# Optimization experiments

Measured on AMD Instinct MI355X. Metric: run time of the kernel, lower is better.

## Reference

```python
import jax, jax.numpy as jnp
import numpy as np

N, E = 50000, 800000
IN = OUT = 128
T, R, H = 4, 6, 8
DK = OUT // H


def setup_inputs() -> dict:
    key = jax.random.key(0)
    ks = iter(jax.random.split(key, 24))
    nk = lambda: next(ks)
    return {
        "node_inp": jax.random.normal(nk(), (N, IN), jnp.float32),
        "node_type": jax.random.randint(nk(), (N,), 0, T),
        "edge_index": jax.random.randint(nk(), (2, E), 0, N),
        "edge_type": jax.random.randint(nk(), (E,), 0, R),
        "edge_sign": jax.random.randint(nk(), (E,), -2, 2),
        "edge_distance": jax.random.uniform(nk(), (E,), jnp.float32, 0.0, 2e5),
        "Wq": jax.random.normal(nk(), (T, IN, OUT), jnp.float32) / np.float32(np.sqrt(IN)),
        "bq": jnp.zeros((T, OUT), jnp.float32),
        "Wk": jax.random.normal(nk(), (T, IN, OUT), jnp.float32) / np.float32(np.sqrt(IN)),
        "bk": jnp.zeros((T, OUT), jnp.float32),
        "Wv": jax.random.normal(nk(), (T, IN, OUT), jnp.float32) / np.float32(np.sqrt(IN)),
        "bv": jnp.zeros((T, OUT), jnp.float32),
        "rel_q": jax.random.normal(nk(), (R, H, DK), jnp.float32) * 0.2,
        "rel_k": jax.random.normal(nk(), (R, H, DK), jnp.float32) * 0.2,
        "rel_v": jax.random.normal(nk(), (R, H, DK), jnp.float32) * 0.2,
        "sign_k_neutral": jnp.ones((H, DK), jnp.float32),
        "sign_v_neutral": jnp.ones((H, DK), jnp.float32),
        "rel_bias": jnp.zeros((R, H), jnp.float32),
        "dist_alpha": jnp.asarray(0.5, jnp.float32),
        "dist_tau": jnp.asarray(100000.0, jnp.float32),
        "skip": jnp.ones((T,), jnp.float32),
        "ln_gamma": jnp.ones((T, OUT), jnp.float32),
        "ln_beta": jnp.zeros((T, OUT), jnp.float32),
    }


def reference(node_inp, node_type, edge_index, edge_type, edge_sign, edge_distance,
              Wq, bq, Wk, bk, Wv, bv, rel_q, rel_k, rel_v,
              sign_k_neutral, sign_v_neutral, rel_bias, dist_alpha, dist_tau,
              skip, ln_gamma, ln_beta):
    n = node_inp.shape[0]
    src, dst = edge_index[0], edge_index[1]

    # edge_sign normalization: anything < -1 or == 0 -> -2 (neutral), else clamp to {-1, 1}
    es = jnp.where((edge_sign < -1) | (edge_sign == 0), -2, jnp.clip(edge_sign, -1, 1))
    sign_idx = jnp.where(es == -1, 0, jnp.where(es == 1, 1, 2))  # [E]

    # per-type Q/K/V projections, then select by node_type
    idx = jnp.arange(n)
    Q = (jnp.einsum('ni,tio->tno', node_inp, Wq) + bq[:, None, :])[node_type, idx]
    K = (jnp.einsum('ni,tio->tno', node_inp, Wk) + bk[:, None, :])[node_type, idx]
    V = (jnp.einsum('ni,tio->tno', node_inp, Wv) + bv[:, None, :])[node_type, idx]
    Q = Q.reshape(n, H, DK); K = K.reshape(n, H, DK); V = V.reshape(n, H, DK)

    sign_k_all = jnp.concatenate([-jnp.ones((1, H, DK), Q.dtype), jnp.ones((1, H, DK), Q.dtype), sign_k_neutral[None]], 0)
    sign_v_all = jnp.concatenate([-jnp.ones((1, H, DK), Q.dtype), jnp.ones((1, H, DK), Q.dtype), sign_v_neutral[None]], 0)

    q_eff = Q[dst] * rel_q[edge_type]                        # [E,H,DK]
    k_eff = K[src] * rel_k[edge_type] * sign_k_all[sign_idx]  # [E,H,DK]
    v_eff = V[src] * rel_v[edge_type] * sign_v_all[sign_idx]  # [E,H,DK]

    scores = (q_eff * k_eff).sum(-1) / np.float32(np.sqrt(DK))  # [E,H]
    scores = scores + rel_bias[edge_type]
    phi = dist_alpha * jnp.exp(-edge_distance / (dist_tau + 1e-9))
    scores = scores + phi[:, None]

    # destination-grouped softmax over edges
    m = jax.ops.segment_max(scores, dst, num_segments=n)      # [N,H]
    ex = jnp.exp(scores - m[dst])
    Z = jax.ops.segment_sum(ex, dst, num_segments=n)          # [N,H]
    attn = ex / (Z[dst] + 1e-9)                               # [E,H]

    msg = (v_eff * attn[..., None]).reshape(-1, OUT)          # [E,OUT]
    out = jax.ops.segment_sum(msg, dst, num_segments=n)       # [N,OUT]

    alpha = jax.nn.sigmoid(skip)[node_type][:, None]          # [N,1]
    mix = alpha * out + (1.0 - alpha) * node_inp
    mu = mix.mean(-1, keepdims=True)
    var = ((mix - mu) ** 2).mean(-1, keepdims=True)
    normed = (mix - mu) / jnp.sqrt(var + 1e-5)
    return normed * ln_gamma[node_type] + ln_beta[node_type]
```

## Files before the change

### kernel.cpp

```cpp
#include <hip/hip_runtime.h>

#define N_NODES 50000
#define N_EDGES 800000
#define DIM 128
#define NT 4
#define NR 6
#define NH 8
#define NBLK_SCAN ((N_NODES + 255) / 256)
#define NTILE_ROW 3129
#define NPAD_MAX (NTILE_ROW * 16)

#define XCVT_N (N_NODES * DIM / 4)
#define WT_N   (NT * 3 * DIM * DIM)
#define WCB_N  (24 * 32)
#define PREP_TOTAL (XCVT_N + WT_N + WCB_N)
#define PREP_BLOCKS ((PREP_TOTAL + 255) / 256)
#define HIST_BLOCKS (N_EDGES / 256)
#define MID_PREP_BASE NBLK_SCAN
#define MID_HIST_BASE (NBLK_SCAN + PREP_BLOCKS)
#define MID_BLOCKS (MID_HIST_BASE + HIST_BLOCKS)

typedef __attribute__((ext_vector_type(8))) short bf16x8;
typedef __attribute__((ext_vector_type(4))) float f32x4;

__device__ __forceinline__ unsigned short f2bf(float f) {
    unsigned int u = __float_as_uint(f);
    return (unsigned short)((u + 0x7fffu + ((u >> 16) & 1u)) >> 16);
}
__device__ __forceinline__ float blo(unsigned int u) { return __uint_as_float(u << 16); }
__device__ __forceinline__ float bhi(unsigned int u) { return __uint_as_float(u & 0xffff0000u); }

__device__ __forceinline__ int sign_index(int s) {
    if (s < -1 || s == 0) return 2;
    return (s == -1) ? 0 : 1;
}

__global__ __launch_bounds__(256) void k_typehist(const int* __restrict__ ntype,
                                                  int* __restrict__ bhist,
                                                  int* __restrict__ cnt,
                                                  int* __restrict__ opad) {
    __shared__ int h[NT];
    if (threadIdx.x < NT) h[threadIdx.x] = 0;
    __syncthreads();
    int n = blockIdx.x * 256 + threadIdx.x;
    if (n < N_NODES) { atomicAdd(&h[ntype[n]], 1); cnt[n] = 0; }
    if (n < NPAD_MAX) opad[n] = -1;
    __syncthreads();
    if (threadIdx.x < NT) bhist[blockIdx.x * NT + threadIdx.x] = h[threadIdx.x];
}

__global__ __launch_bounds__(1024) void k_typescan(const int* __restrict__ bhist,
                                                   int* __restrict__ bbase,
                                                   int* __restrict__ pb_g) {
    __shared__ int s[1024];
    __shared__ int pb[NT + 1];
    int tid = threadIdx.x;
    int t = tid / NBLK_SCAN;
    int b = tid - t * NBLK_SCAN;
    int v = (tid < NT * NBLK_SCAN) ? bhist[b * NT + t] : 0;
    s[tid] = v;
    __syncthreads();
    for (int d = 1; d < 1024; d <<= 1) {
        int add = (tid >= d) ? s[tid - d] : 0;
        __syncthreads();
        s[tid] += add;
        __syncthreads();
    }
    if (tid == 0) {
        int acc = 0;
        for (int tt = 0; tt < NT; ++tt) {
            pb[tt] = acc;
            int tot = s[(tt + 1) * NBLK_SCAN - 1] - (tt ? s[tt * NBLK_SCAN - 1] : 0);
            acc += ((tot + 15) >> 4) << 4;
        }
        pb[NT] = acc;
    }
    __syncthreads();
    if (tid < NT * NBLK_SCAN) {
        int excl = s[tid] - v;
        int base_t = t ? s[t * NBLK_SCAN - 1] : 0;
        bbase[b * NT + t] = pb[t] + (excl - base_t);
    }
    if (tid <= NT) pb_g[tid] = pb[tid];
}

__global__ __launch_bounds__(256) void k_mid(
    const int* __restrict__ ntype, const int* __restrict__ bbase, int* __restrict__ order_pad,
    const float* __restrict__ x,
    const float* __restrict__ Wq, const float* __restrict__ Wk, const float* __restrict__ Wv,
    const float* __restrict__ rel_q, const float* __restrict__ rel_k,
    const float* __restrict__ rel_v,
    const float* __restrict__ skn, const float* __restrict__ svn,
    unsigned short* __restrict__ xb, unsigned short* __restrict__ Wt,
    uint4* __restrict__ wcb,
    const int* __restrict__ ei, int* __restrict__ cnt, int* __restrict__ posw)
{
    int blk = blockIdx.x;
    if (blk < NBLK_SCAN) {
        __shared__ int cur[NT];
        if (threadIdx.x < NT) cur[threadIdx.x] = bbase[blk * NT + threadIdx.x];
        __syncthreads();
        int n = blk * 256 + threadIdx.x;
        if (n < N_NODES) {
            int t = ntype[n];
            int pos = atomicAdd(&cur[t], 1);
            order_pad[pos] = n;
        }
        return;
    }
    if (blk < MID_HIST_BASE) {
        int i = (blk - MID_PREP_BASE) * 256 + threadIdx.x;
        if (i < XCVT_N) {
            float4 v = ((const float4*)x)[i];
            ushort4 o;
            o.x = f2bf(v.x); o.y = f2bf(v.y); o.z = f2bf(v.z); o.w = f2bf(v.w);
            ((ushort4*)xb)[i] = o;
        } else if (i < XCVT_N + WT_N) {
            int j = i - XCVT_N;
            int in = j & 127;
            int b2 = j >> 7;
            int out = b2 & 127;
            int ts = b2 >> 7;
            int sel = ts % 3, t = ts / 3;
            const float* W = sel == 0 ? Wq : (sel == 1 ? Wk : Wv);
            Wt[j] = f2bf(W[((size_t)t * DIM + in) * DIM + out]);
        } else if (i < PREP_TOTAL) {
            int j = i - XCVT_N - WT_N;
            int p = j & 31;
            int cmb = j >> 5;
            int et = cmb & 7, sidx = cmb >> 3;
            if (et < NR) {
                int h = p >> 2;
                float wk[4], wv[4];
                #pragma unroll
                for (int q = 0; q < 4; ++q) {
                    int o = 4 * p + q;
                    int rb = (et * NH + h) * 16 + (o & 15);
                    float sgk = sidx == 0 ? -1.f : (sidx == 1 ? 1.f : skn[o]);
                    float sgv = sidx == 0 ? -1.f : (sidx == 1 ? 1.f : svn[o]);
                    wk[q] = rel_q[rb] * rel_k[rb] * sgk * 0.25f;
                    wv[q] = rel_v[rb] * sgv;
                }
                uint4 u;
                u.x = (unsigned)f2bf(wk[0]) | ((unsigned)f2bf(wk[1]) << 16);
                u.y = (unsigned)f2bf(wv[0]) | ((unsigned)f2bf(wv[1]) << 16);
                u.z = (unsigned)f2bf(wk[2]) | ((unsigned)f2bf(wk[3]) << 16);
                u.w = (unsigned)f2bf(wv[2]) | ((unsigned)f2bf(wv[3]) << 16);
                wcb[cmb * 32 + p] = u;
            }
        }
        return;
    }
    int e = (blk - MID_HIST_BASE) * 256 + threadIdx.x;
    if (e < N_EDGES) posw[e] = atomicAdd(&cnt[ei[N_EDGES + e]], 1);
}

__global__ __launch_bounds__(256) void k_projm(
    const unsigned short* __restrict__ xb, const unsigned short* __restrict__ Wt,
    const int* __restrict__ order_pad, const int* __restrict__ pb_g,
    const float* __restrict__ bq, const float* __restrict__ bk, const float* __restrict__ bv,
    float* __restrict__ Qf, unsigned short* __restrict__ KVu,
    const int* __restrict__ cnt, int* __restrict__ offs, int* __restrict__ bsum)
{
    int b = blockIdx.x;
    if (b >= NTILE_ROW) {
        int sb = b - NTILE_ROW;
        __shared__ int s[256];
        int i = sb * 256 + threadIdx.x;
        int v = (i < N_NODES) ? cnt[i] : 0;
        s[threadIdx.x] = v;
        __syncthreads();
        for (int d = 1; d < 256; d <<= 1) {
            int add = (threadIdx.x >= d) ? s[threadIdx.x - d] : 0;
            __syncthreads();
            s[threadIdx.x] += add;
            __syncthreads();
        }
        if (i < N_NODES) offs[i] = s[threadIdx.x] - v;
        if (threadIdx.x == 255) bsum[sb] = s[255];
        return;
    }
    int row0 = b * 16;
    if (row0 >= pb_g[NT]) return;
    int t = (row0 >= pb_g[3]) ? 3 : (row0 >= pb_g[2]) ? 2 : (row0 >= pb_g[1]) ? 1 : 0;
    int wave = threadIdx.x >> 6, lane = threadIdx.x & 63;
    int arow = row0 + (lane & 15);
    int nidA = order_pad[arow];
    const unsigned short* xrow = xb + (size_t)(nidA < 0 ? 0 : nidA) * DIM;
    int ko = (lane >> 4) * 8;
    bf16x8 afrag[4];
    #pragma unroll
    for (int kt = 0; kt < 4; ++kt) afrag[kt] = *(const bf16x8*)(xrow + kt * 32 + ko);

    #pragma unroll
    for (int g = 0; g < 6; ++g) {
        int ocol = g * 64 + wave * 16 + (lane & 15);
        int sel = ocol >> 7, wcol = ocol & 127;
        const unsigned short* wrow = Wt + ((size_t)(t * 3 + sel) * DIM + wcol) * DIM;
        f32x4 acc = {0.f, 0.f, 0.f, 0.f};
        #pragma unroll
        for (int kt = 0; kt < 4; ++kt) {
            bf16x8 bfr = *(const bf16x8*)(wrow + kt * 32 + ko);
            acc = __builtin_amdgcn_mfma_f32_16x16x32_bf16(afrag[kt], bfr, acc, 0, 0, 0);
        }
        const float* bias_p = sel == 0 ? bq : (sel == 1 ? bk : bv);
        float bias = bias_p[t * DIM + wcol];
        #pragma unroll
        for (int r = 0; r < 4; ++r) {
            int drow = row0 + (lane >> 4) * 4 + r;
            int nid = order_pad[drow];
            if (nid < 0) continue;
            float v = acc[r] + bias;
            if (sel == 0) Qf[(size_t)nid * DIM + wcol] = v;
            else KVu[(size_t)nid * 256 + (wcol >> 1) * 4 + (wcol & 1) + (sel == 2 ? 2 : 0)] = f2bf(v);
        }
    }
}

__global__ __launch_bounds__(256) void k_scan2(const int* __restrict__ bsum,
                                               int* __restrict__ bofs, int* __restrict__ offs) {
    __shared__ int s[256];
    int t = threadIdx.x;
    int v = (t < NBLK_SCAN) ? bsum[t] : 0;
    s[t] = v;
    __syncthreads();
    for (int d = 1; d < 256; d <<= 1) {
        int add = (t >= d) ? s[t - d] : 0;
        __syncthreads();
        s[t] += add;
        __syncthreads();
    }
    if (t < NBLK_SCAN) {
        int b = s[t] - v;
        bofs[t] = b;
        if (t == NBLK_SCAN - 1) offs[N_NODES] = N_EDGES - b;
    }
}

__global__ void k_emit(const int* __restrict__ ei, const int* __restrict__ etype,
                       const int* __restrict__ esign, const float* __restrict__ edist,
                       const float* __restrict__ dalpha, const float* __restrict__ dtau,
                       const int* __restrict__ offs, const int* __restrict__ bofs,
                       const int* __restrict__ posw, int2* __restrict__ edata) {
    int e = blockIdx.x * blockDim.x + threadIdx.x;
    if (e >= N_EDGES) return;
    int dst = ei[N_EDGES + e];
    int pos = offs[dst] + bofs[dst >> 8] + posw[e];
    int cmb = sign_index(esign[e]) * 8 + etype[e];
    float phi = dalpha[0] * __expf(-edist[e] / (dtau[0] + 1e-9f));
    edata[pos] = make_int2(ei[e] | (cmb << 16), __float_as_int(phi));
}

__global__ __launch_bounds__(256) void k_attn(
    const float4* __restrict__ Qf4, const uint4* __restrict__ KV,
    const uint4* __restrict__ WCB,
    const float* __restrict__ x, const int* __restrict__ ntype,
    const int* __restrict__ offs, const int* __restrict__ bofs,
    const int2* __restrict__ edata,
    const float* __restrict__ rbias, const float* __restrict__ skip,
    const float* __restrict__ gmm, const float* __restrict__ bta,
    float* __restrict__ out)
{
    __shared__ float rb_s[NR * NH];
    if (threadIdx.x < NR * NH) rb_s[threadIdx.x] = rbias[threadIdx.x];
    __syncthreads();
    const int wave = threadIdx.x >> 6, lane = threadIdx.x & 63;
    const int n = blockIdx.x * 4 + wave;
    const int p = lane & 31;
    const int hi = lane >> 5;
    const int h = p >> 2;
    const int beg = offs[n] + bofs[n >> 8];
    const int end = offs[n + 1] + bofs[(n + 1) >> 8];

    const float4 q4 = Qf4[(size_t)n * 32 + p];

    float Z = 0.f, a0 = 0.f, a1 = 0.f, a2 = 0.f, a3 = 0.f;

    auto process = [&](int2 r) {
        int src = r.x & 0xffff;
        unsigned cmb = ((unsigned)r.x) >> 16;
        uint4 kv = KV[(size_t)src * 32 + p];
        uint4 w = WCB[cmb * 32 + p];
        float pp = (q4.x * blo(w.x)) * blo(kv.x);
        pp = fmaf(q4.y * bhi(w.x), bhi(kv.x), pp);
        pp = fmaf(q4.z * blo(w.z), blo(kv.z), pp);
        pp = fmaf(q4.w * bhi(w.z), bhi(kv.z), pp);
        pp += __shfl_xor(pp, 1, 4);
        pp += __shfl_xor(pp, 2, 4);
        float ex = __expf(pp + rb_s[(cmb & 7) * NH + h] + __int_as_float(r.y));
        Z += ex;
        a0 = fmaf(blo(kv.y) * blo(w.y), ex, a0);
        a1 = fmaf(bhi(kv.y) * bhi(w.y), ex, a1);
        a2 = fmaf(blo(kv.w) * blo(w.w), ex, a2);
        a3 = fmaf(bhi(kv.w) * bhi(w.w), ex, a3);
    };

    int rem = end - beg;
    int j = beg;
    if (rem >= 4) {
        int2 r0 = edata[j + hi];
        int2 r1 = edata[j + 2 + hi];
        while (true) {
            int2 c0 = r0, c1 = r1;
            j += 4; rem -= 4;
            if (rem >= 4) { r0 = edata[j + hi]; r1 = edata[j + 2 + hi]; }
            process(c0);
            process(c1);
            if (rem < 4) break;
        }
    }
    while (rem >= 2) {
        int2 c = edata[j + hi];
        process(c);
        j += 2; rem -= 2;
    }
    if (rem) {
        int2 r = edata[j];
        int src = r.x & 0xffff;
        unsigned cmb = ((unsigned)r.x) >> 16;
        uint4 kv = KV[(size_t)src * 32 + p];
        uint4 w = WCB[cmb * 32 + p];
        float pp = (q4.x * blo(w.x)) * blo(kv.x);
        pp = fmaf(q4.y * bhi(w.x), bhi(kv.x), pp);
        pp = fmaf(q4.z * blo(w.z), blo(kv.z), pp);
        pp = fmaf(q4.w * bhi(w.z), bhi(kv.z), pp);
        pp += __shfl_xor(pp, 1, 4);
        pp += __shfl_xor(pp, 2, 4);
        float ex = __expf(pp + rb_s[(cmb & 7) * NH + h] + __int_as_float(r.y));
        ex = hi ? 0.f : ex;
        Z += ex;
        a0 = fmaf(blo(kv.y) * blo(w.y), ex, a0);
        a1 = fmaf(bhi(kv.y) * bhi(w.y), ex, a1);
        a2 = fmaf(blo(kv.w) * blo(w.w), ex, a2);
        a3 = fmaf(bhi(kv.w) * bhi(w.w), ex, a3);
    }

    Z  += __shfl_xor(Z, 32, 64);
    a0 += __shfl_xor(a0, 32, 64);
    a1 += __shfl_xor(a1, 32, 64);
    a2 += __shfl_xor(a2, 32, 64);
    a3 += __shfl_xor(a3, 32, 64);

    float rz = 1.f / (Z + 1e-9f);
    int t = ntype[n];
    float alpha = 1.f / (1.f + __expf(-skip[t]));
    float4 x4 = ((const float4*)x)[(size_t)n * 32 + p];
    float m0 = fmaf(alpha, a0 * rz - x4.x, x4.x);
    float m1 = fmaf(alpha, a1 * rz - x4.y, x4.y);
    float m2 = fmaf(alpha, a2 * rz - x4.z, x4.z);
    float m3 = fmaf(alpha, a3 * rz - x4.w, x4.w);

    float s = (m0 + m1) + (m2 + m3);
    float s2 = fmaf(m0, m0, m1 * m1) + fmaf(m2, m2, m3 * m3);
    #pragma unroll
    for (int d = 32; d >= 1; d >>= 1) {
        s += __shfl_xor(s, d, 64);
        s2 += __shfl_xor(s2, d, 64);
    }
    float mu = s * (1.f / (2 * DIM));
    float var = s2 * (1.f / (2 * DIM)) - mu * mu;
    float rstd = rsqrtf(var + 1e-5f);
    if (hi == 0) {
        float4 g4 = ((const float4*)gmm)[t * 32 + p];
        float4 b4 = ((const float4*)bta)[t * 32 + p];
        float4 o4;
        o4.x = (m0 - mu) * rstd * g4.x + b4.x;
        o4.y = (m1 - mu) * rstd * g4.y + b4.y;
        o4.z = (m2 - mu) * rstd * g4.z + b4.z;
        o4.w = (m3 - mu) * rstd * g4.w + b4.w;
        ((float4*)out)[(size_t)n * 32 + p] = o4;
    }
}

extern "C" void kernel_launch(void* const* d_in, const int* in_sizes, int n_in,
                              void* d_out, int out_size, void* d_ws, size_t ws_size,
                              hipStream_t stream) {
    const float* x      = (const float*)d_in[0];
    const int*   ntype  = (const int*)d_in[1];
    const int*   ei     = (const int*)d_in[2];
    const int*   etype  = (const int*)d_in[3];
    const int*   esign  = (const int*)d_in[4];
    const float* edist  = (const float*)d_in[5];
    const float* Wq     = (const float*)d_in[6];
    const float* bq     = (const float*)d_in[7];
    const float* Wk     = (const float*)d_in[8];
    const float* bk     = (const float*)d_in[9];
    const float* Wv     = (const float*)d_in[10];
    const float* bv     = (const float*)d_in[11];
    const float* rel_q  = (const float*)d_in[12];
    const float* rel_k  = (const float*)d_in[13];
    const float* rel_v  = (const float*)d_in[14];
    const float* skn    = (const float*)d_in[15];
    const float* svn    = (const float*)d_in[16];
    const float* rbias  = (const float*)d_in[17];
    const float* dalpha = (const float*)d_in[18];
    const float* dtau   = (const float*)d_in[19];
    const float* skip   = (const float*)d_in[20];
    const float* gmm    = (const float*)d_in[21];
    const float* bta    = (const float*)d_in[22];
    float* out = (float*)d_out;

    char* ws = (char*)d_ws;
    float*          Qf     = (float*)         (ws + 0);
    unsigned short* KVu    = (unsigned short*)(ws + 25600000);
    unsigned short* xb     = (unsigned short*)(ws + 51200000);
    unsigned short* Wt     = (unsigned short*)(ws + 64000000);
    uint4*          wcb    = (uint4*)         (ws + 64500000);
    int*            cnt    = (int*)           (ws + 64600000);
    int*            offs   = (int*)           (ws + 64900000);
    int*            bsum   = (int*)           (ws + 65200000);
    int*            bofs   = (int*)           (ws + 65210000);
    int*            posw   = (int*)           (ws + 65300000);
    int2*           edata  = (int2*)          (ws + 68600000);
    int*            opad   = (int*)           (ws + 75000000);
    int*            bhist  = (int*)           (ws + 75300000);
    int*            bbase  = (int*)           (ws + 75310000);
    int*            pb     = (int*)           (ws + 75320000);

    k_typehist <<<NBLK_SCAN, 256, 0, stream>>>(ntype, bhist, cnt, opad);
    k_typescan <<<1, 1024, 0, stream>>>(bhist, bbase, pb);
    k_mid <<<MID_BLOCKS, 256, 0, stream>>>(ntype, bbase, opad,
                                           x, Wq, Wk, Wv, rel_q, rel_k, rel_v, skn, svn,
                                           xb, Wt, wcb,
                                           ei, cnt, posw);
    k_projm <<<NTILE_ROW + NBLK_SCAN, 256, 0, stream>>>(xb, Wt, opad, pb, bq, bk, bv,
                                                        Qf, KVu, cnt, offs, bsum);
    k_scan2 <<<1, 256, 0, stream>>>(bsum, bofs, offs);
    k_emit <<<HIST_BLOCKS, 256, 0, stream>>>(ei, etype, esign, edist, dalpha, dtau,
                                             offs, bofs, posw, edata);
    k_attn <<<N_NODES / 4, 256, 0, stream>>>((const float4*)Qf, (const uint4*)KVu,
                                             (const uint4*)wcb, x, ntype, offs, bofs,
                                             edata, rbias, skip, gmm, bta, out);
}
```

Baseline: 182.8 us.

## Prefetch gathered KV rows in attention loop, split relation weights to fp32, restructure projection GEMM

The attention kernel now issues the gathered KV and relation-weight loads for the next pair of edges before processing the current pair, so memory latency overlaps with compute. The combined relation/sign weight table is split into separate fp32 K and V tables, which removes bf16 unpacking but doubles that table's footprint and load count. The projection GEMM is reorganized so each block owns one output-column group and loops over a chunk of 8 row tiles. Weight fragments are reused across tiles and reloaded only when the node type changes, while x rows are now re-read for each of the 6 column groups.

```diff
diff --git a/kernel.cpp b/kernel.cpp
--- a/kernel.cpp
+++ b/kernel.cpp
@@ -9,6 +9,9 @@
 #define NBLK_SCAN ((N_NODES + 255) / 256)
 #define NTILE_ROW 3129
 #define NPAD_MAX (NTILE_ROW * 16)
+#define CHUNK 8
+#define NCHUNK ((NTILE_ROW + CHUNK - 1) / CHUNK)
+#define GEMM_BLOCKS (NCHUNK * 6)
 
 #define XCVT_N (N_NODES * DIM / 4)
 #define WT_N   (NT * 3 * DIM * DIM)
@@ -92,7 +95,7 @@
     const float* __restrict__ rel_v,
     const float* __restrict__ skn, const float* __restrict__ svn,
     unsigned short* __restrict__ xb, unsigned short* __restrict__ Wt,
-    uint4* __restrict__ wcb,
+    float4* __restrict__ wcbK, float4* __restrict__ wcbV,
     const int* __restrict__ ei, int* __restrict__ cnt, int* __restrict__ posw)
 {
     int blk = blockIdx.x;
@@ -141,12 +144,8 @@
                     wk[q] = rel_q[rb] * rel_k[rb] * sgk * 0.25f;
                     wv[q] = rel_v[rb] * sgv;
                 }
-                uint4 u;
-                u.x = (unsigned)f2bf(wk[0]) | ((unsigned)f2bf(wk[1]) << 16);
-                u.y = (unsigned)f2bf(wv[0]) | ((unsigned)f2bf(wv[1]) << 16);
-                u.z = (unsigned)f2bf(wk[2]) | ((unsigned)f2bf(wk[3]) << 16);
-                u.w = (unsigned)f2bf(wv[2]) | ((unsigned)f2bf(wv[3]) << 16);
-                wcb[cmb * 32 + p] = u;
+                wcbK[cmb * 32 + p] = make_float4(wk[0], wk[1], wk[2], wk[3]);
+                wcbV[cmb * 32 + p] = make_float4(wv[0], wv[1], wv[2], wv[3]);
             }
         }
         return;
@@ -163,8 +162,8 @@
     const int* __restrict__ cnt, int* __restrict__ offs, int* __restrict__ bsum)
 {
     int b = blockIdx.x;
-    if (b >= NTILE_ROW) {
-        int sb = b - NTILE_ROW;
+    if (b >= GEMM_BLOCKS) {
+        int sb = b - GEMM_BLOCKS;
         __shared__ int s[256];
         int i = sb * 256 + threadIdx.x;
         int v = (i < N_NODES) ? cnt[i] : 0;
@@ -180,31 +179,38 @@
         if (threadIdx.x == 255) bsum[sb] = s[255];
         return;
     }
-    int row0 = b * 16;
-    if (row0 >= pb_g[NT]) return;
-    int t = (row0 >= pb_g[3]) ? 3 : (row0 >= pb_g[2]) ? 2 : (row0 >= pb_g[1]) ? 1 : 0;
+    int chunk = b / 6, g = b % 6;
     int wave = threadIdx.x >> 6, lane = threadIdx.x & 63;
-    int arow = row0 + (lane & 15);
-    int nidA = order_pad[arow];
-    const unsigned short* xrow = xb + (size_t)(nidA < 0 ? 0 : nidA) * DIM;
+    int ocol = g * 64 + wave * 16 + (lane & 15);
+    int sel = ocol >> 7, wcol = ocol & 127;
     int ko = (lane >> 4) * 8;
-    bf16x8 afrag[4];
-    #pragma unroll
-    for (int kt = 0; kt < 4; ++kt) afrag[kt] = *(const bf16x8*)(xrow + kt * 32 + ko);
-
-    #pragma unroll
-    for (int g = 0; g < 6; ++g) {
-        int ocol = g * 64 + wave * 16 + (lane & 15);
-        int sel = ocol >> 7, wcol = ocol & 127;
-        const unsigned short* wrow = Wt + ((size_t)(t * 3 + sel) * DIM + wcol) * DIM;
+    const float* bias_p = sel == 0 ? bq : (sel == 1 ? bk : bv);
+    int cur_t = -1;
+    bf16x8 bfr[4];
+    float bias = 0.f;
+    int tile0 = chunk * CHUNK;
+    int tmax = pb_g[NT];
+    #pragma unroll 1
+    for (int tt = 0; tt < CHUNK; ++tt) {
+        int row0 = (tile0 + tt) * 16;
+        if (row0 >= tmax) break;
+        int t = (row0 >= pb_g[3]) ? 3 : (row0 >= pb_g[2]) ? 2 : (row0 >= pb_g[1]) ? 1 : 0;
+        if (t != cur_t) {
+            cur_t = t;
+            const unsigned short* wrow = Wt + ((size_t)(t * 3 + sel) * DIM + wcol) * DIM;
+            #pragma unroll
+            for (int kt = 0; kt < 4; ++kt) bfr[kt] = *(const bf16x8*)(wrow + kt * 32 + ko);
+            bias = bias_p[t * DIM + wcol];
+        }
+        int arow = row0 + (lane & 15);
+        int nidA = order_pad[arow];
+        const unsigned short* xrow = xb + (size_t)(nidA < 0 ? 0 : nidA) * DIM;
         f32x4 acc = {0.f, 0.f, 0.f, 0.f};
         #pragma unroll
         for (int kt = 0; kt < 4; ++kt) {
-            bf16x8 bfr = *(const bf16x8*)(wrow + kt * 32 + ko);
-            acc = __builtin_amdgcn_mfma_f32_16x16x32_bf16(afrag[kt], bfr, acc, 0, 0, 0);
-        }
-        const float* bias_p = sel == 0 ? bq : (sel == 1 ? bk : bv);
-        float bias = bias_p[t * DIM + wcol];
+            bf16x8 a = *(const bf16x8*)(xrow + kt * 32 + ko);
+            acc = __builtin_amdgcn_mfma_f32_16x16x32_bf16(a, bfr[kt], acc, 0, 0, 0);
+        }
         #pragma unroll
         for (int r = 0; r < 4; ++r) {
             int drow = row0 + (lane >> 4) * 4 + r;
@@ -253,7 +259,7 @@
 
 __global__ __launch_bounds__(256) void k_attn(
     const float4* __restrict__ Qf4, const uint4* __restrict__ KV,
-    const uint4* __restrict__ WCB,
+    const float4* __restrict__ WK, const float4* __restrict__ WV,
     const float* __restrict__ x, const int* __restrict__ ntype,
     const int* __restrict__ offs, const int* __restrict__ bofs,
     const int2* __restrict__ edata,
@@ -276,63 +282,77 @@
 
     float Z = 0.f, a0 = 0.f, a1 = 0.f, a2 = 0.f, a3 = 0.f;
 
-    auto process = [&](int2 r) {
-        int src = r.x & 0xffff;
-        unsigned cmb = ((unsigned)r.x) >> 16;
-        uint4 kv = KV[(size_t)src * 32 + p];
-        uint4 w = WCB[cmb * 32 + p];
-        float pp = (q4.x * blo(w.x)) * blo(kv.x);
-        pp = fmaf(q4.y * bhi(w.x), bhi(kv.x), pp);
-        pp = fmaf(q4.z * blo(w.z), blo(kv.z), pp);
-        pp = fmaf(q4.w * bhi(w.z), bhi(kv.z), pp);
+    auto PROC = [&](int2 r, uint4 kv, float4 wk, float4 wv) {
+        float pp = (q4.x * wk.x) * blo(kv.x);
+        pp = fmaf(q4.y * wk.y, bhi(kv.x), pp);
+        pp = fmaf(q4.z * wk.z, blo(kv.z), pp);
+        pp = fmaf(q4.w * wk.w, bhi(kv.z), pp);
         pp += __shfl_xor(pp, 1, 4);
         pp += __shfl_xor(pp, 2, 4);
+        unsigned cmb = ((unsigned)r.x) >> 16;
         float ex = __expf(pp + rb_s[(cmb & 7) * NH + h] + __int_as_float(r.y));
         Z += ex;
-        a0 = fmaf(blo(kv.y) * blo(w.y), ex, a0);
-        a1 = fmaf(bhi(kv.y) * bhi(w.y), ex, a1);
-        a2 = fmaf(blo(kv.w) * blo(w.w), ex, a2);
-        a3 = fmaf(bhi(kv.w) * bhi(w.w), ex, a3);
+        a0 = fmaf(blo(kv.y) * wv.x, ex, a0);
+        a1 = fmaf(bhi(kv.y) * wv.y, ex, a1);
+        a2 = fmaf(blo(kv.w) * wv.z, ex, a2);
+        a3 = fmaf(bhi(kv.w) * wv.w, ex, a3);
     };
 
     int rem = end - beg;
     int j = beg;
     if (rem >= 4) {
-        int2 r0 = edata[j + hi];
-        int2 r1 = edata[j + 2 + hi];
-        while (true) {
-            int2 c0 = r0, c1 = r1;
+        int2 r0 = edata[j + hi], r1 = edata[j + 2 + hi];
+        uint4  kv0 = KV[(size_t)(r0.x & 0xffff) * 32 + p];
+        float4 wk0 = WK[(((unsigned)r0.x) >> 16) * 32 + p];
+        float4 wv0 = WV[(((unsigned)r0.x) >> 16) * 32 + p];
+        uint4  kv1 = KV[(size_t)(r1.x & 0xffff) * 32 + p];
+        float4 wk1 = WK[(((unsigned)r1.x) >> 16) * 32 + p];
+        float4 wv1 = WV[(((unsigned)r1.x) >> 16) * 32 + p];
+        while (rem >= 8) {
+            int2 n0 = edata[j + 4 + hi], n1 = edata[j + 6 + hi];
+            uint4  nkv0 = KV[(size_t)(n0.x & 0xffff) * 32 + p];
+            float4 nwk0 = WK[(((unsigned)n0.x) >> 16) * 32 + p];
+            float4 nwv0 = WV[(((unsigned)n0.x) >> 16) * 32 + p];
+            uint4  nkv1 = KV[(size_t)(n1.x & 0xffff) * 32 + p];
+            float4 nwk1 = WK[(((unsigned)n1.x) >> 16) * 32 + p];
+            float4 nwv1 = WV[(((unsigned)n1.x) >> 16) * 32 + p];
+            PROC(r0, kv0, wk0, wv0);
+            PROC(r1, kv1, wk1, wv1);
+            r0 = n0; kv0 = nkv0; wk0 = nwk0; wv0 = nwv0;
+            r1 = n1; kv1 = nkv1; wk1 = nwk1; wv1 = nwv1;
             j += 4; rem -= 4;
-            if (rem >= 4) { r0 = edata[j + hi]; r1 = edata[j + 2 + hi]; }
-            process(c0);
-            process(c1);
-            if (rem < 4) break;
-        }
+        }
+        PROC(r0, kv0, wk0, wv0);
+        PROC(r1, kv1, wk1, wv1);
+        j += 4; rem -= 4;
     }
     while (rem >= 2) {
-        int2 c = edata[j + hi];
-        process(c);
+        int2 r = edata[j + hi];
+        uint4  kv = KV[(size_t)(r.x & 0xffff) * 32 + p];
+        float4 wk = WK[(((unsigned)r.x) >> 16) * 32 + p];
+        float4 wv = WV[(((unsigned)r.x) >> 16) * 32 + p];
+        PROC(r, kv, wk, wv);
         j += 2; rem -= 2;
     }
     if (rem) {
         int2 r = edata[j];
-        int src = r.x & 0xffff;
-        unsigned cmb = ((unsigned)r.x) >> 16;
-        uint4 kv = KV[(size_t)src * 32 + p];
-        uint4 w = WCB[cmb * 32 + p];
-        float pp = (q4.x * blo(w.x)) * blo(kv.x);
-        pp = fmaf(q4.y * bhi(w.x), bhi(kv.x), pp);
-        pp = fmaf(q4.z * blo(w.z), blo(kv.z), pp);
-        pp = fmaf(q4.w * bhi(w.z), bhi(kv.z), pp);
+        uint4  kv = KV[(size_t)(r.x & 0xffff) * 32 + p];
+        float4 wk = WK[(((unsigned)r.x) >> 16) * 32 + p];
+        float4 wv = WV[(((unsigned)r.x) >> 16) * 32 + p];
+        float pp = (q4.x * wk.x) * blo(kv.x);
+        pp = fmaf(q4.y * wk.y, bhi(kv.x), pp);
+        pp = fmaf(q4.z * wk.z, blo(kv.z), pp);
+        pp = fmaf(q4.w * wk.w, bhi(kv.z), pp);
         pp += __shfl_xor(pp, 1, 4);
         pp += __shfl_xor(pp, 2, 4);
+        unsigned cmb = ((unsigned)r.x) >> 16;
         float ex = __expf(pp + rb_s[(cmb & 7) * NH + h] + __int_as_float(r.y));
         ex = hi ? 0.f : ex;
         Z += ex;
-        a0 = fmaf(blo(kv.y) * blo(w.y), ex, a0);
-        a1 = fmaf(bhi(kv.y) * bhi(w.y), ex, a1);
-        a2 = fmaf(blo(kv.w) * blo(w.w), ex, a2);
-        a3 = fmaf(bhi(kv.w) * bhi(w.w), ex, a3);
+        a0 = fmaf(blo(kv.y) * wv.x, ex, a0);
+        a1 = fmaf(bhi(kv.y) * wv.y, ex, a1);
+        a2 = fmaf(blo(kv.w) * wv.z, ex, a2);
+        a3 = fmaf(bhi(kv.w) * wv.w, ex, a3);
     }
 
     Z  += __shfl_xor(Z, 32, 64);
@@ -405,7 +425,8 @@
     unsigned short* KVu    = (unsigned short*)(ws + 25600000);
     unsigned short* xb     = (unsigned short*)(ws + 51200000);
     unsigned short* Wt     = (unsigned short*)(ws + 64000000);
-    uint4*          wcb    = (uint4*)         (ws + 64500000);
+    float4*         wcbK   = (float4*)        (ws + 64500000);
+    float4*         wcbV   = (float4*)        (ws + 64520000);
     int*            cnt    = (int*)           (ws + 64600000);
     int*            offs   = (int*)           (ws + 64900000);
     int*            bsum   = (int*)           (ws + 65200000);
@@ -421,14 +442,15 @@
     k_typescan <<<1, 1024, 0, stream>>>(bhist, bbase, pb);
     k_mid <<<MID_BLOCKS, 256, 0, stream>>>(ntype, bbase, opad,
                                            x, Wq, Wk, Wv, rel_q, rel_k, rel_v, skn, svn,
-                                           xb, Wt, wcb,
+                                           xb, Wt, wcbK, wcbV,
                                            ei, cnt, posw);
-    k_projm <<<NTILE_ROW + NBLK_SCAN, 256, 0, stream>>>(xb, Wt, opad, pb, bq, bk, bv,
-                                                        Qf, KVu, cnt, offs, bsum);
+    k_projm <<<GEMM_BLOCKS + NBLK_SCAN, 256, 0, stream>>>(xb, Wt, opad, pb, bq, bk, bv,
+                                                          Qf, KVu, cnt, offs, bsum);
     k_scan2 <<<1, 256, 0, stream>>>(bsum, bofs, offs);
     k_emit <<<HIST_BLOCKS, 256, 0, stream>>>(ei, etype, esign, edist, dalpha, dtau,
                                              offs, bofs, posw, edata);
     k_attn <<<N_NODES / 4, 256, 0, stream>>>((const float4*)Qf, (const uint4*)KVu,
-                                             (const uint4*)wcb, x, ntype, offs, bofs,
+                                             (const float4*)wcbK, (const float4*)wcbV,
+                                             x, ntype, offs, bofs,
                                              edata, rbias, skip, gmm, bta, out);
 }
```

After: 199.2 us. 1.09x slower.

## Regroup preprocessing stages into fewer fused launches to cut kernel launch count

Applied to the files above, without the earlier changes.

Restructures the preprocessing pipeline so independent stages share launches: the type histogram joins the conversion/edge-count kernel, the type scan and per-node offset scan share one kernel, the type scatter and block-sum scan share another, and the edge emit runs alongside the projection GEMM. The node-count scan switches to 1024-thread blocks so the second-level scan covers fewer blocks, and the count buffer is cleared with a memset. This is meant to remove launch gaps and tiny serial kernels, at the cost of more heterogeneous blocks within each launch.

```diff
diff --git a/kernel.cpp b/kernel.cpp
--- a/kernel.cpp
+++ b/kernel.cpp
@@ -7,6 +7,7 @@
 #define NR 6
 #define NH 8
 #define NBLK_SCAN ((N_NODES + 255) / 256)
+#define NBLK2 ((N_NODES + 1023) / 1024)
 #define NTILE_ROW 3129
 #define NPAD_MAX (NTILE_ROW * 16)
 
@@ -16,9 +17,9 @@
 #define PREP_TOTAL (XCVT_N + WT_N + WCB_N)
 #define PREP_BLOCKS ((PREP_TOTAL + 255) / 256)
 #define HIST_BLOCKS (N_EDGES / 256)
-#define MID_PREP_BASE NBLK_SCAN
-#define MID_HIST_BASE (NBLK_SCAN + PREP_BLOCKS)
-#define MID_BLOCKS (MID_HIST_BASE + HIST_BLOCKS)
+#define A_PREP_BASE NBLK_SCAN
+#define A_HIST_BASE (NBLK_SCAN + PREP_BLOCKS)
+#define A_BLOCKS (A_HIST_BASE + HIST_BLOCKS)
 
 typedef __attribute__((ext_vector_type(8))) short bf16x8;
 typedef __attribute__((ext_vector_type(4))) float f32x4;
@@ -35,57 +36,8 @@
     return (s == -1) ? 0 : 1;
 }
 
-__global__ __launch_bounds__(256) void k_typehist(const int* __restrict__ ntype,
-                                                  int* __restrict__ bhist,
-                                                  int* __restrict__ cnt,
-                                                  int* __restrict__ opad) {
-    __shared__ int h[NT];
-    if (threadIdx.x < NT) h[threadIdx.x] = 0;
-    __syncthreads();
-    int n = blockIdx.x * 256 + threadIdx.x;
-    if (n < N_NODES) { atomicAdd(&h[ntype[n]], 1); cnt[n] = 0; }
-    if (n < NPAD_MAX) opad[n] = -1;
-    __syncthreads();
-    if (threadIdx.x < NT) bhist[blockIdx.x * NT + threadIdx.x] = h[threadIdx.x];
-}
-
-__global__ __launch_bounds__(1024) void k_typescan(const int* __restrict__ bhist,
-                                                   int* __restrict__ bbase,
-                                                   int* __restrict__ pb_g) {
-    __shared__ int s[1024];
-    __shared__ int pb[NT + 1];
-    int tid = threadIdx.x;
-    int t = tid / NBLK_SCAN;
-    int b = tid - t * NBLK_SCAN;
-    int v = (tid < NT * NBLK_SCAN) ? bhist[b * NT + t] : 0;
-    s[tid] = v;
-    __syncthreads();
-    for (int d = 1; d < 1024; d <<= 1) {
-        int add = (tid >= d) ? s[tid - d] : 0;
-        __syncthreads();
-        s[tid] += add;
-        __syncthreads();
-    }
-    if (tid == 0) {
-        int acc = 0;
-        for (int tt = 0; tt < NT; ++tt) {
-            pb[tt] = acc;
-            int tot = s[(tt + 1) * NBLK_SCAN - 1] - (tt ? s[tt * NBLK_SCAN - 1] : 0);
-            acc += ((tot + 15) >> 4) << 4;
-        }
-        pb[NT] = acc;
-    }
-    __syncthreads();
-    if (tid < NT * NBLK_SCAN) {
-        int excl = s[tid] - v;
-        int base_t = t ? s[t * NBLK_SCAN - 1] : 0;
-        bbase[b * NT + t] = pb[t] + (excl - base_t);
-    }
-    if (tid <= NT) pb_g[tid] = pb[tid];
-}
-
-__global__ __launch_bounds__(256) void k_mid(
-    const int* __restrict__ ntype, const int* __restrict__ bbase, int* __restrict__ order_pad,
+__global__ __launch_bounds__(256) void k_A(
+    const int* __restrict__ ntype, int* __restrict__ bhist, int* __restrict__ opad,
     const float* __restrict__ x,
     const float* __restrict__ Wq, const float* __restrict__ Wk, const float* __restrict__ Wv,
     const float* __restrict__ rel_q, const float* __restrict__ rel_k,
@@ -97,19 +49,18 @@
 {
     int blk = blockIdx.x;
     if (blk < NBLK_SCAN) {
-        __shared__ int cur[NT];
-        if (threadIdx.x < NT) cur[threadIdx.x] = bbase[blk * NT + threadIdx.x];
+        __shared__ int h[NT];
+        if (threadIdx.x < NT) h[threadIdx.x] = 0;
         __syncthreads();
         int n = blk * 256 + threadIdx.x;
-        if (n < N_NODES) {
-            int t = ntype[n];
-            int pos = atomicAdd(&cur[t], 1);
-            order_pad[pos] = n;
-        }
+        if (n < N_NODES) atomicAdd(&h[ntype[n]], 1);
+        if (n < NPAD_MAX) opad[n] = -1;
+        __syncthreads();
+        if (threadIdx.x < NT) bhist[blk * NT + threadIdx.x] = h[threadIdx.x];
         return;
     }
-    if (blk < MID_HIST_BASE) {
-        int i = (blk - MID_PREP_BASE) * 256 + threadIdx.x;
+    if (blk < A_HIST_BASE) {
+        int i = (blk - A_PREP_BASE) * 256 + threadIdx.x;
         if (i < XCVT_N) {
             float4 v = ((const float4*)x)[i];
             ushort4 o;
@@ -130,12 +81,12 @@
             int cmb = j >> 5;
             int et = cmb & 7, sidx = cmb >> 3;
             if (et < NR) {
-                int h = p >> 2;
+                int h2 = p >> 2;
                 float wk[4], wv[4];
                 #pragma unroll
                 for (int q = 0; q < 4; ++q) {
                     int o = 4 * p + q;
-                    int rb = (et * NH + h) * 16 + (o & 15);
+                    int rb = (et * NH + h2) * 16 + (o & 15);
                     float sgk = sidx == 0 ? -1.f : (sidx == 1 ? 1.f : skn[o]);
                     float sgv = sidx == 0 ? -1.f : (sidx == 1 ? 1.f : svn[o]);
                     wk[q] = rel_q[rb] * rel_k[rb] * sgk * 0.25f;
@@ -151,33 +102,118 @@
         }
         return;
     }
-    int e = (blk - MID_HIST_BASE) * 256 + threadIdx.x;
+    int e = (blk - A_HIST_BASE) * 256 + threadIdx.x;
     if (e < N_EDGES) posw[e] = atomicAdd(&cnt[ei[N_EDGES + e]], 1);
 }
 
-__global__ __launch_bounds__(256) void k_projm(
+__global__ __launch_bounds__(1024) void k_B(
+    const int* __restrict__ bhist, int* __restrict__ bbase, int* __restrict__ pb_g,
+    const int* __restrict__ cnt, int* __restrict__ offs, int* __restrict__ bsum)
+{
+    int tid = threadIdx.x;
+    if (blockIdx.x == 0) {
+        __shared__ int s[1024];
+        __shared__ int pb[NT + 1];
+        int t = tid / NBLK_SCAN;
+        int b = tid - t * NBLK_SCAN;
+        int v = (tid < NT * NBLK_SCAN) ? bhist[b * NT + t] : 0;
+        s[tid] = v;
+        __syncthreads();
+        for (int d = 1; d < 1024; d <<= 1) {
+            int add = (tid >= d) ? s[tid - d] : 0;
+            __syncthreads();
+            s[tid] += add;
+            __syncthreads();
+        }
+        if (tid == 0) {
+            int acc = 0;
+            for (int tt = 0; tt < NT; ++tt) {
+                pb[tt] = acc;
+                int tot = s[(tt + 1) * NBLK_SCAN - 1] - (tt ? s[tt * NBLK_SCAN - 1] : 0);
+                acc += ((tot + 15) >> 4) << 4;
+            }
+            pb[NT] = acc;
+        }
+        __syncthreads();
+        if (tid < NT * NBLK_SCAN) {
+            int excl = s[tid] - v;
+            int base_t = t ? s[t * NBLK_SCAN - 1] : 0;
+            bbase[b * NT + t] = pb[t] + (excl - base_t);
+        }
+        if (tid <= NT) pb_g[tid] = pb[tid];
+        return;
+    }
+    int sb = blockIdx.x - 1;
+    __shared__ int s[1024];
+    int i = sb * 1024 + tid;
+    int v = (i < N_NODES) ? cnt[i] : 0;
+    s[tid] = v;
+    __syncthreads();
+    for (int d = 1; d < 1024; d <<= 1) {
+        int add = (tid >= d) ? s[tid - d] : 0;
+        __syncthreads();
+        s[tid] += add;
+        __syncthreads();
+    }
+    if (i < N_NODES) offs[i] = s[tid] - v;
+    if (tid == 1023) bsum[sb] = s[1023];
+}
+
+__global__ __launch_bounds__(256) void k_C(
+    const int* __restrict__ ntype, const int* __restrict__ bbase, int* __restrict__ order_pad,
+    const int* __restrict__ bsum, int* __restrict__ bofs, int* __restrict__ offs)
+{
+    int blk = blockIdx.x;
+    if (blk < NBLK_SCAN) {
+        __shared__ int cur[NT];
+        if (threadIdx.x < NT) cur[threadIdx.x] = bbase[blk * NT + threadIdx.x];
+        __syncthreads();
+        int n = blk * 256 + threadIdx.x;
+        if (n < N_NODES) {
+            int t = ntype[n];
+            int pos = atomicAdd(&cur[t], 1);
+            order_pad[pos] = n;
+        }
+        return;
+    }
+    __shared__ int s[256];
+    int t = threadIdx.x;
+    int v = (t < NBLK2) ? bsum[t] : 0;
+    s[t] = v;
+    __syncthreads();
+    for (int d = 1; d < 256; d <<= 1) {
+        int add = (t >= d) ? s[t - d] : 0;
+        __syncthreads();
+        s[t] += add;
+        __syncthreads();
+    }
+    if (t < NBLK2) {
+        int b = s[t] - v;
+        bofs[t] = b;
+        if (t == NBLK2 - 1) offs[N_NODES] = N_EDGES - b;
+    }
+}
+
+__global__ __launch_bounds__(256) void k_D(
     const unsigned short* __restrict__ xb, const unsigned short* __restrict__ Wt,
     const int* __restrict__ order_pad, const int* __restrict__ pb_g,
     const float* __restrict__ bq, const float* __restrict__ bk, const float* __restrict__ bv,
     float* __restrict__ Qf, unsigned short* __restrict__ KVu,
-    const int* __restrict__ cnt, int* __restrict__ offs, int* __restrict__ bsum)
+    const int* __restrict__ ei, const int* __restrict__ etype,
+    const int* __restrict__ esign, const float* __restrict__ edist,
+    const float* __restrict__ dalpha, const float* __restrict__ dtau,
+    const int* __restrict__ offs, const int* __restrict__ bofs,
+    const int* __restrict__ posw, int2* __restrict__ edata)
 {
     int b = blockIdx.x;
     if (b >= NTILE_ROW) {
-        int sb = b - NTILE_ROW;
-        __shared__ int s[256];
-        int i = sb * 256 + threadIdx.x;
-        int v = (i < N_NODES) ? cnt[i] : 0;
-        s[threadIdx.x] = v;
-        __syncthreads();
-        for (int d = 1; d < 256; d <<= 1) {
-            int add = (threadIdx.x >= d) ? s[threadIdx.x - d] : 0;
-            __syncthreads();
-            s[threadIdx.x] += add;
-            __syncthreads();
-        }
-        if (i < N_NODES) offs[i] = s[threadIdx.x] - v;
-        if (threadIdx.x == 255) bsum[sb] = s[255];
+        int e = (b - NTILE_ROW) * 256 + threadIdx.x;
+        if (e >= N_EDGES) return;
+        int dst = ei[N_EDGES + e];
+        int pos = offs[dst] + bofs[dst >> 10] + posw[e];
+        int cmb = sign_index(esign[e]) * 8 + etype[e];
+        float phi = dalpha[0] * __expf(-edist[e] / (dtau[0] + 1e-9f));
+        edata[pos] = make_int2(ei[e] | (cmb << 16), __float_as_int(phi));
         return;
     }
     int row0 = b * 16;
@@ -215,40 +251,6 @@
             else KVu[(size_t)nid * 256 + (wcol >> 1) * 4 + (wcol & 1) + (sel == 2 ? 2 : 0)] = f2bf(v);
         }
     }
-}
-
-__global__ __launch_bounds__(256) void k_scan2(const int* __restrict__ bsum,
-                                               int* __restrict__ bofs, int* __restrict__ offs) {
-    __shared__ int s[256];
-    int t = threadIdx.x;
-    int v = (t < NBLK_SCAN) ? bsum[t] : 0;
-    s[t] = v;
-    __syncthreads();
-    for (int d = 1; d < 256; d <<= 1) {
-        int add = (t >= d) ? s[t - d] : 0;
-        __syncthreads();
-        s[t] += add;
-        __syncthreads();
-    }
-    if (t < NBLK_SCAN) {
-        int b = s[t] - v;
-        bofs[t] = b;
-        if (t == NBLK_SCAN - 1) offs[N_NODES] = N_EDGES - b;
-    }
-}
-
-__global__ void k_emit(const int* __restrict__ ei, const int* __restrict__ etype,
-                       const int* __restrict__ esign, const float* __restrict__ edist,
-                       const float* __restrict__ dalpha, const float* __restrict__ dtau,
-                       const int* __restrict__ offs, const int* __restrict__ bofs,
-                       const int* __restrict__ posw, int2* __restrict__ edata) {
-    int e = blockIdx.x * blockDim.x + threadIdx.x;
-    if (e >= N_EDGES) return;
-    int dst = ei[N_EDGES + e];
-    int pos = offs[dst] + bofs[dst >> 8] + posw[e];
-    int cmb = sign_index(esign[e]) * 8 + etype[e];
-    float phi = dalpha[0] * __expf(-edist[e] / (dtau[0] + 1e-9f));
-    edata[pos] = make_int2(ei[e] | (cmb << 16), __float_as_int(phi));
 }
 
 __global__ __launch_bounds__(256) void k_attn(
@@ -269,8 +271,8 @@
     const int p = lane & 31;
     const int hi = lane >> 5;
     const int h = p >> 2;
-    const int beg = offs[n] + bofs[n >> 8];
-    const int end = offs[n + 1] + bofs[(n + 1) >> 8];
+    const int beg = offs[n] + bofs[n >> 10];
+    const int end = offs[n + 1] + bofs[(n + 1) >> 10];
 
     const float4 q4 = Qf4[(size_t)n * 32 + p];
 
@@ -417,17 +419,16 @@
     int*            bbase  = (int*)           (ws + 75310000);
     int*            pb     = (int*)           (ws + 75320000);
 
-    k_typehist <<<NBLK_SCAN, 256, 0, stream>>>(ntype, bhist, cnt, opad);
-    k_typescan <<<1, 1024, 0, stream>>>(bhist, bbase, pb);
-    k_mid <<<MID_BLOCKS, 256, 0, stream>>>(ntype, bbase, opad,
-                                           x, Wq, Wk, Wv, rel_q, rel_k, rel_v, skn, svn,
-                                           xb, Wt, wcb,
-                                           ei, cnt, posw);
-    k_projm <<<NTILE_ROW + NBLK_SCAN, 256, 0, stream>>>(xb, Wt, opad, pb, bq, bk, bv,
-                                                        Qf, KVu, cnt, offs, bsum);
-    k_scan2 <<<1, 256, 0, stream>>>(bsum, bofs, offs);
-    k_emit <<<HIST_BLOCKS, 256, 0, stream>>>(ei, etype, esign, edist, dalpha, dtau,
-                                             offs, bofs, posw, edata);
+    hipMemsetAsync(cnt, 0, (size_t)N_NODES * 4, stream);
+    k_A <<<A_BLOCKS, 256, 0, stream>>>(ntype, bhist, opad,
+                                       x, Wq, Wk, Wv, rel_q, rel_k, rel_v, skn, svn,
+                                       xb, Wt, wcb, ei, cnt, posw);
+    k_B <<<1 + NBLK2, 1024, 0, stream>>>(bhist, bbase, pb, cnt, offs, bsum);
+    k_C <<<NBLK_SCAN + 1, 256, 0, stream>>>(ntype, bbase, opad, bsum, bofs, offs);
+    k_D <<<NTILE_ROW + HIST_BLOCKS, 256, 0, stream>>>(xb, Wt, opad, pb, bq, bk, bv,
+                                                      Qf, KVu,
+                                                      ei, etype, esign, edist, dalpha, dtau,
+                                                      offs, bofs, posw, edata);
     k_attn <<<N_NODES / 4, 256, 0, stream>>>((const float4*)Qf, (const uint4*)KVu,
                                              (const uint4*)wcb, x, ntype, offs, bofs,
                                              edata, rbias, skip, gmm, bta, out);
```

Result: faster. 175.3 us (-4.1%).
